# Kernel optimization log

Measured on AMD Instinct MI355X. Metric: run time of the kernel, lower is better.

The kernel has to match this reference:

```python
import jax, jax.numpy as jnp
import numpy as np


def _gat(x, adj, W, a):
    # x: [N, J, Fin], W: [H, Fin, hs], a: [H, 2*hs]
    # e_ij = leakyrelu(a1.Wh_i + a2.Wh_j)  (decomposed form of the repeat/cat construction)
    hs = W.shape[-1]
    Wh = jnp.einsum('bjf,hfd->bhjd', x, W)
    s1 = jnp.einsum('bhjd,hd->bhj', Wh, a[:, :hs])
    s2 = jnp.einsum('bhjd,hd->bhj', Wh, a[:, hs:])
    e = jax.nn.leaky_relu(s1[..., :, None] + s2[..., None, :], 0.2)
    e = jnp.where(adj[None, None] > 0, e, jnp.float32(-9e15))
    att = jax.nn.softmax(e, axis=-1)
    h = jnp.einsum('bhij,bhjd->bhid', att, Wh)
    b, H, j, d = h.shape
    return jax.nn.elu(h.transpose(0, 2, 1, 3).reshape(b, j, H * d))


def _conv_bn_relu(x, w, bias, g, be, m, v):
    # x: [N, C, T], w: [O, I, 3], BN in inference mode
    y = jax.lax.conv_general_dilated(x, w, (1,), [(1, 1)], dimension_numbers=('NCH', 'OIH', 'NCH'))
    y = y + bias[None, :, None]
    y = (y - m[None, :, None]) / jnp.sqrt(v[None, :, None] + 1e-5) * g[None, :, None] + be[None, :, None]
    return jax.nn.relu(y)


def _mha(q, k, v, wq, bq, wk, bk, wv, bv, wo, bo):
    # torch nn.MultiheadAttention, 4 heads, eval mode (no dropout)
    n, L, D = q.shape
    H = 4
    hd = D // H
    def proj(x, w, b):
        return (x @ w.T + b).reshape(n, -1, H, hd)
    Q, K, V = proj(q, wq, bq), proj(k, wk, bk), proj(v, wv, bv)
    att = jax.nn.softmax(jnp.einsum('nqhd,nkhd->nhqk', Q, K) * jnp.float32(1.0 / np.sqrt(hd)), axis=-1)
    o = jnp.einsum('nhqk,nkhd->nqhd', att, V).reshape(n, L, D)
    return o @ wo.T + bo


def _lstm_dir(x, wih, whh, bih, bhh, rev):
    # x: [B, T, D]; torch gate order i, f, g, o
    b, t, _ = x.shape
    H = whh.shape[1]
    xw = jnp.transpose(x @ wih.T + (bih + bhh), (1, 0, 2))  # [T, B, 4H]
    def step(carry, xt):
        h, c = carry
        gates = xt + h @ whh.T
        i, f, g, o = jnp.split(gates, 4, axis=-1)
        c = jax.nn.sigmoid(f) * c + jax.nn.sigmoid(i) * jnp.tanh(g)
        h = jax.nn.sigmoid(o) * jnp.tanh(c)
        return (h, c), h
    init = (jnp.zeros((b, H), x.dtype), jnp.zeros((b, H), x.dtype))
    _, hs = jax.lax.scan(step, init, xw, reverse=rev)
    return jnp.transpose(hs, (1, 0, 2))


def _forward(lh, rh, adj, vis, g1W, g1a, g2W, g2a, c1w, c1b, b1g, b1b, b1m, b1v, c2w, c2b, b2g, b2b, b2m, b2v,
             wq, bq, wk, bk, wv, bv, wo, bo,
             l0fw, l0fu, l0fbi, l0fbh, l0bw, l0bu, l0bbi, l0bbh,
             l1fw, l1fu, l1fbi, l1fbh, l1bw, l1bu, l1bbi, l1bbh,
             o1w, o1b, o2w, o2b):
    B, T, J, F = lh.shape

    def single_hand(x):
        h = x.reshape(B * T, J, F)
        h = _gat(h, adj, g1W, g1a)
        h = _gat(h, adj, g2W, g2a)
        D = h.shape[-1]
        ht = h.reshape(B, T, J, D).transpose(0, 2, 3, 1).reshape(B * J, D, T)
        ht = _conv_bn_relu(ht, c1w, c1b, b1g, b1b, b1m, b1v)
        ht = _conv_bn_relu(ht, c2w, c2b, b2g, b2b, b2m, b2v)
        return ht.reshape(B, J, D, T).transpose(0, 3, 1, 2)  # [B, T, J, D]

    l = single_hand(lh)
    r = single_hand(rh)
    D = l.shape[-1]
    lf = l.reshape(B * T, J, D)
    rf = r.reshape(B * T, J, D)
    a_l2r = _mha(lf, rf, rf, wq, bq, wk, bk, wv, bv, wo, bo)
    a_r2l = _mha(rf, lf, lf, wq, bq, wk, bk, wv, bv, wo, bo)
    # repair of shape-inconsistent torch reshape: pool joints before the seq LSTM
    le = (lf + 0.5 * a_r2l).reshape(B, T, J, D).mean(axis=2)
    re = (rf + 0.5 * a_l2r).reshape(B, T, J, D).mean(axis=2)

    def bilstm(x):
        h1 = jnp.concatenate([_lstm_dir(x, l0fw, l0fu, l0fbi, l0fbh, False),
                              _lstm_dir(x, l0bw, l0bu, l0bbi, l0bbh, True)], -1)
        return jnp.concatenate([_lstm_dir(h1, l1fw, l1fu, l1fbi, l1fbh, False),
                                _lstm_dir(h1, l1bw, l1bu, l1bbi, l1bbh, True)], -1)

    def head(x):
        y = jax.nn.relu(x @ o1w.T + o1b) @ o2w.T + o2b  # [B, T, 3*J]
        return y.reshape(B, T, J, 3)

    lp = head(bilstm(le)) * vis[..., None]
    rp = head(bilstm(re)) * vis[..., None]
    return lp, rp


def setup_inputs() -> dict:
    key = jax.random.key(0)
    ks = jax.random.split(key, 60)
    it = iter(range(60))
    B, T, J, F, D = 8, 512, 21, 512, 256
    def nrm(shape, s=0.05):
        return jax.random.normal(ks[next(it)], shape, jnp.float32) * s
    inp = {}
    inp['left_hand_feats'] = nrm((B, T, J, F), 1.0)
    inp['right_hand_feats'] = nrm((B, T, J, F), 1.0)
    adj = (jax.random.uniform(ks[next(it)], (J, J)) < 0.3).astype(jnp.float32)
    inp['hand_adj_matrix'] = jnp.maximum(adj, jnp.eye(J, dtype=jnp.float32))
    inp['hand_visibility'] = jax.random.uniform(ks[next(it)], (B, T, J), jnp.float32)
    inp['gat1_W'] = nrm((4, F, 64)); inp['gat1_a'] = nrm((4, 128))
    inp['gat2_W'] = nrm((4, D, 64)); inp['gat2_a'] = nrm((4, 128))
    inp['conv1_w'] = nrm((D, D, 3)); inp['conv1_b'] = nrm((D,))
    inp['conv2_w'] = nrm((D, D, 3)); inp['conv2_b'] = nrm((D,))
    for p in ['bn1', 'bn2']:
        inp[p + '_g'] = jnp.ones((D,), jnp.float32)
        inp[p + '_b'] = jnp.zeros((D,), jnp.float32)
        inp[p + '_m'] = jnp.zeros((D,), jnp.float32)
        inp[p + '_v'] = jnp.ones((D,), jnp.float32)
    for p in ['attn_wq', 'attn_wk', 'attn_wv', 'attn_wo']:
        inp[p] = nrm((D, D))
    for p in ['attn_bq', 'attn_bk', 'attn_bv', 'attn_bo']:
        inp[p] = nrm((D,))
    H = D // 2
    for l in ['lstm0f', 'lstm0b', 'lstm1f', 'lstm1b']:
        inp[l + '_wih'] = nrm((4 * H, D))
        inp[l + '_whh'] = nrm((4 * H, H))
        inp[l + '_bih'] = nrm((4 * H,))
        inp[l + '_bhh'] = nrm((4 * H,))
    inp['out1_w'] = nrm((D, D)); inp['out1_b'] = nrm((D,))
    inp['out2_w'] = nrm((3 * J, D)); inp['out2_b'] = nrm((3 * J,))
    return inp


def reference(left_hand_feats, right_hand_feats, hand_adj_matrix, hand_visibility,
              gat1_W, gat1_a, gat2_W, gat2_a,
              conv1_w, conv1_b, bn1_g, bn1_b, bn1_m, bn1_v,
              conv2_w, conv2_b, bn2_g, bn2_b, bn2_m, bn2_v,
              attn_wq, attn_bq, attn_wk, attn_bk, attn_wv, attn_bv, attn_wo, attn_bo,
              lstm0f_wih, lstm0f_whh, lstm0f_bih, lstm0f_bhh,
              lstm0b_wih, lstm0b_whh, lstm0b_bih, lstm0b_bhh,
              lstm1f_wih, lstm1f_whh, lstm1f_bih, lstm1f_bhh,
              lstm1b_wih, lstm1b_whh, lstm1b_bih, lstm1b_bhh,
              out1_w, out1_b, out2_w, out2_b):
    return _forward(left_hand_feats, right_hand_feats, hand_adj_matrix, hand_visibility,
                    gat1_W, gat1_a, gat2_W, gat2_a,
                    conv1_w, conv1_b, bn1_g, bn1_b, bn1_m, bn1_v,
                    conv2_w, conv2_b, bn2_g, bn2_b, bn2_m, bn2_v,
                    attn_wq, attn_bq, attn_wk, attn_bk, attn_wv, attn_bv, attn_wo, attn_bo,
                    lstm0f_wih, lstm0f_whh, lstm0f_bih, lstm0f_bhh,
                    lstm0b_wih, lstm0b_whh, lstm0b_bih, lstm0b_bhh,
                    lstm1f_wih, lstm1f_whh, lstm1f_bih, lstm1f_bhh,
                    lstm1b_wih, lstm1b_whh, lstm1b_bih, lstm1b_bhh,
                    out1_w, out1_b, out2_w, out2_b)
```

## Files before the change

kernel.cpp:

```cpp
#include <hip/hip_runtime.h>

typedef __bf16 bf16;
typedef bf16 bf16x8 __attribute__((ext_vector_type(8)));
typedef bf16 bf16x4 __attribute__((ext_vector_type(4)));
typedef float f32x4 __attribute__((ext_vector_type(4)));
typedef _Float16 f16;
typedef f16 f16x8 __attribute__((ext_vector_type(8)));

#define NBT 4096
#define NJ 21
#define NLF 86016
#define DD 256
#define CONV_M 86352
#define SPAD 514
#define CROWS 86528

__device__ __forceinline__ void gload16(const bf16* g, bf16* l) {
  __builtin_amdgcn_global_load_lds(
      (const __attribute__((address_space(1))) unsigned int*)g,
      (__attribute__((address_space(3))) unsigned int*)l, 16, 0, 0);
}

__global__ __launch_bounds__(256, 2) void gemm_bf16(
    const void* __restrict__ Av, const bf16* __restrict__ Bt,
    float* __restrict__ C32, bf16* __restrict__ Cout,
    const float* __restrict__ bias, const float* __restrict__ sc,
    const float* __restrict__ sh, int M, int N, int K, int lda, int flags)
{
  __shared__ __align__(16) bf16 As[128][32];
  __shared__ __align__(16) bf16 Bs[128][32];
  const int tid = threadIdx.x;
  const long m0 = (long)blockIdx.y * 128;
  const int n0 = blockIdx.x * 128;
  const int wave = tid >> 6, lane = tid & 63;
  const int wm = (wave & 1) * 64, wn = (wave >> 1) * 64;
  const int frow = lane & 15, fkb = (lane >> 4) * 8;
  const int crow = lane >> 2, ccol = (lane & 3) * 8;
  f32x4 acc[4][4] = {};
  for (int k0 = 0; k0 < K; k0 += 32) {
    if (flags & 1) {
      const int lr = tid >> 1, lc = (tid & 1) * 16;
      const float* ap = (const float*)Av + (m0 + lr) * (long)lda + (k0 + lc);
      bf16x8 t0, t1;
      #pragma unroll
      for (int u = 0; u < 8; u++) { t0[u] = (bf16)ap[u]; t1[u] = (bf16)ap[8 + u]; }
      *(bf16x8*)(&As[lr][lc])     = t0;
      *(bf16x8*)(&As[lr][lc + 8]) = t1;
    } else {
      #pragma unroll
      for (int cc = 0; cc < 2; cc++) {
        const int ch = wave * 2 + cc;
        gload16((const bf16*)Av + (m0 + ch * 16 + crow) * (long)lda + (k0 + ccol),
                &As[ch * 16][0]);
      }
    }
    #pragma unroll
    for (int cc = 0; cc < 2; cc++) {
      const int ch = wave * 2 + cc;
      gload16(Bt + (n0 + ch * 16 + crow) * (long)K + (k0 + ccol),
              &Bs[ch * 16][0]);
    }
    __syncthreads();
    bf16x8 af[4], bg[4];
    #pragma unroll
    for (int i = 0; i < 4; i++) af[i] = *(const bf16x8*)(&As[wm + i * 16 + frow][fkb]);
    #pragma unroll
    for (int j = 0; j < 4; j++) bg[j] = *(const bf16x8*)(&Bs[wn + j * 16 + frow][fkb]);
    #pragma unroll
    for (int i = 0; i < 4; i++)
      #pragma unroll
      for (int j = 0; j < 4; j++)
        acc[i][j] = __builtin_amdgcn_mfma_f32_16x16x32_bf16(af[i], bg[j], acc[i][j], 0, 0, 0);
    __syncthreads();
  }
  const int col = lane & 15, rbase = (lane >> 4) * 4;
  #pragma unroll
  for (int i = 0; i < 4; i++) {
    #pragma unroll
    for (int j = 0; j < 4; j++) {
      const int nn = n0 + wn + j * 16 + col;
      #pragma unroll
      for (int r = 0; r < 4; r++) {
        const long mm = m0 + wm + i * 16 + rbase + r;
        if (mm >= M) continue;
        float v = acc[i][j][r];
        if (flags & 2) { C32[mm * (long)N + nn] = v; continue; }
        if (flags & 8) v = v * sc[nn] + sh[nn];
        else if (bias) v += bias[nn];
        if (flags & 4) v = fmaxf(v, 0.f);
        if (flags & 16) {
          const int s = (int)(mm % SPAD);
          if (s == 0 || s == SPAD - 1) v = 0.f;
          Cout[mm * (long)N + nn] = (bf16)v;
        } else if (flags & 32) {
          const long hj = mm / SPAD; const int s = (int)(mm - hj * SPAD);
          if (s == 0 || s == SPAD - 1) continue;
          const long b = hj / NJ; const int j2 = (int)(hj - b * NJ);
          const long dst = (b * 512 + (s - 1)) * NJ + j2;
          Cout[dst * (long)N + nn] = (bf16)v;
        } else {
          Cout[mm * (long)N + nn] = (bf16)v;
        }
      }
    }
  }
}

__global__ void cvt_k(const float* __restrict__ s, bf16* __restrict__ d, long n) {
  long i = (long)blockIdx.x * 256 + threadIdx.x;
  if (i < n) d[i] = (bf16)s[i];
}
__global__ void cvt4_k(const float* __restrict__ s, bf16* __restrict__ d, long n4) {
  long i = (long)blockIdx.x * 256 + threadIdx.x;
  if (i >= n4) return;
  const f32x4 v = ((const f32x4*)s)[i];
  bf16x4 o; o[0] = (bf16)v[0]; o[1] = (bf16)v[1]; o[2] = (bf16)v[2]; o[3] = (bf16)v[3];
  ((bf16x4*)d)[i] = o;
}
__global__ void prep_gatW(const float* __restrict__ W, bf16* __restrict__ Wt, int F) {
  long idx = (long)blockIdx.x * 256 + threadIdx.x;
  if (idx >= 256L * F) return;
  int n = (int)(idx / F), f = (int)(idx % F);
  Wt[idx] = (bf16)W[((long)(n >> 6) * F + f) * 64 + (n & 63)];
}
__global__ void prep_convw(const float* __restrict__ w, bf16* __restrict__ wp) {
  int idx = blockIdx.x * 256 + threadIdx.x;
  int n = idx / 768, k = idx % 768, tap = k >> 8, i = k & 255;
  wp[idx] = (bf16)w[(n * 256 + i) * 3 + tap];
}
__global__ void prep_out2(const float* __restrict__ w, bf16* __restrict__ wp) {
  int idx = blockIdx.x * 256 + threadIdx.x;
  wp[idx] = (idx < 63 * 256) ? (bf16)w[idx] : (bf16)0.f;
}
__global__ void prep_scsh(const float* __restrict__ cb, const float* __restrict__ g,
                          const float* __restrict__ be, const float* __restrict__ m,
                          const float* __restrict__ v, float* __restrict__ sc,
                          float* __restrict__ sh) {
  int c = threadIdx.x;
  float rs = rsqrtf(v[c] + 1e-5f) * g[c];
  sc[c] = rs; sh[c] = (cb[c] - m[c]) * rs + be[c];
}
__global__ void pad_zero(bf16* __restrict__ convIn) {
  int idx = blockIdx.x * 256 + threadIdx.x;
  int hj = idx >> 9, s = ((idx >> 8) & 1) ? (SPAD - 1) : 0, c = idx & 255;
  convIn[((long)hj * SPAD + s) * DD + c] = (bf16)0.f;
}
__global__ void zero_out(float* __restrict__ o, long n) {
  long i = (long)blockIdx.x * 256 + threadIdx.x;
  if (i < n) o[i] = 0.f;
}

__global__ __launch_bounds__(256) void gat_attn(
    const bf16* __restrict__ Wh, const float* __restrict__ a,
    const float* __restrict__ adj, bf16* __restrict__ out, int convMode)
{
  const int bt = blockIdx.x, tid = threadIdx.x;
  __shared__ float whs[NJ][DD];
  __shared__ float s1[4][NJ], s2[4][NJ];
  __shared__ float att[4][NJ][NJ];
  const long base = (long)bt * NJ * DD;
  for (int i = tid; i < NJ * DD; i += 256)
    whs[i >> 8][i & 255] = (float)Wh[base + i];
  __syncthreads();
  if (tid < 4 * NJ) {
    const int h = tid / NJ, i = tid % NJ;
    float x1 = 0.f, x2 = 0.f;
    for (int d = 0; d < 64; d++) {
      const float w = whs[i][h * 64 + d];
      x1 += w * a[h * 128 + d];
      x2 += w * a[h * 128 + 64 + d];
    }
    s1[h][i] = x1; s2[h][i] = x2;
  }
  __syncthreads();
  for (int idx = tid; idx < 4 * NJ * NJ; idx += 256) {
    const int h = idx / (NJ * NJ), r = idx % (NJ * NJ), i = r / NJ, j = r % NJ;
    float e = s1[h][i] + s2[h][j];
    e = e > 0.f ? e : 0.2f * e;
    att[h][i][j] = (adj[i * NJ + j] > 0.f) ? e : -9e15f;
  }
  __syncthreads();
  if (tid < 4 * NJ) {
    const int h = tid / NJ, i = tid % NJ;
    float mx = -3e38f;
    for (int j = 0; j < NJ; j++) mx = fmaxf(mx, att[h][i][j]);
    float sum = 0.f;
    for (int j = 0; j < NJ; j++) { const float ex = __expf(att[h][i][j] - mx); att[h][i][j] = ex; sum += ex; }
    const float inv = 1.f / sum;
    for (int j = 0; j < NJ; j++) att[h][i][j] *= inv;
  }
  __syncthreads();
  const int b = bt >> 9, t = bt & 511;
  for (int idx = tid; idx < NJ * DD; idx += 256) {
    const int i = idx >> 8, c = idx & 255, h = c >> 6;
    float s = 0.f;
    for (int j = 0; j < NJ; j++) s += att[h][i][j] * whs[j][c];
    s = s > 0.f ? s : (__expf(s) - 1.f);
    const long row = convMode ? (((long)(b * NJ + i)) * SPAD + (t + 1)) : ((long)bt * NJ + i);
    out[row * DD + c] = (bf16)s;
  }
}

__global__ __launch_bounds__(256) void mha_core(
    const bf16* __restrict__ Q, const bf16* __restrict__ K,
    const bf16* __restrict__ V, bf16* __restrict__ O)
{
  const int bt = blockIdx.x, tid = threadIdx.x;
  __shared__ bf16 qs[NJ][DD], ks[NJ][DD], vs[NJ][DD];
  __shared__ float att[4][NJ][NJ];
  const long base = (long)bt * NJ * DD;
  for (int i = tid; i < NJ * DD; i += 256) {
    const int r = i >> 8, c = i & 255;
    qs[r][c] = Q[base + i]; ks[r][c] = K[base + i]; vs[r][c] = V[base + i];
  }
  __syncthreads();
  for (int idx = tid; idx < 4 * NJ * NJ; idx += 256) {
    const int h = idx / (NJ * NJ), r = idx % (NJ * NJ), i = r / NJ, j = r % NJ;
    float s = 0.f;
    for (int d = 0; d < 64; d++) s += (float)qs[i][h * 64 + d] * (float)ks[j][h * 64 + d];
    att[h][i][j] = s * 0.125f;
  }
  __syncthreads();
  if (tid < 4 * NJ) {
    const int h = tid / NJ, i = tid % NJ;
    float mx = -3e38f;
    for (int j = 0; j < NJ; j++) mx = fmaxf(mx, att[h][i][j]);
    float sum = 0.f;
    for (int j = 0; j < NJ; j++) { const float ex = __expf(att[h][i][j] - mx); att[h][i][j] = ex; sum += ex; }
    const float inv = 1.f / sum;
    for (int j = 0; j < NJ; j++) att[h][i][j] *= inv;
  }
  __syncthreads();
  for (int idx = tid; idx < NJ * DD; idx += 256) {
    const int i = idx >> 8, c = idx & 255, h = c >> 6;
    float s = 0.f;
    for (int j = 0; j < NJ; j++) s += att[h][i][j] * (float)vs[j][c];
    O[base + i * DD + c] = (bf16)s;
  }
}

__global__ __launch_bounds__(256) void pool_kernel(
    const bf16* __restrict__ lf, const bf16* __restrict__ ao, bf16* __restrict__ o)
{
  const int bt = blockIdx.x, c = threadIdx.x;
  float s = 0.f;
  for (int j = 0; j < NJ; j++) {
    const long r = ((long)bt * NJ + j) * DD + c;
    s += (float)lf[r] + 0.5f * (float)ao[r];
  }
  o[(long)bt * DD + c] = (bf16)(s * (1.f / 21.f));
}

#define REP16(X) X(0) X(1) X(2) X(3) X(4) X(5) X(6) X(7) X(8) X(9) X(10) X(11) \
  X(12) X(13) X(14) X(15)

#define LDS_FENCE() do { \
  asm volatile("s_waitcnt lgkmcnt(0)" ::: "memory"); \
  __builtin_amdgcn_sched_barrier(0); \
  __builtin_amdgcn_s_barrier(); \
  __builtin_amdgcn_sched_barrier(0); \
} while (0)

__global__ __launch_bounds__(512, 1) void lstm_lds(
    const float* __restrict__ xw,
    const float* __restrict__ whhF, const float* __restrict__ whhB,
    const float* __restrict__ bihF, const float* __restrict__ bhhF,
    const float* __restrict__ bihB, const float* __restrict__ bhhB,
    bf16* __restrict__ outL, bf16* __restrict__ outR)
{
  const int wg = blockIdx.x;
  const int hand = wg >> 4, dir = (wg >> 3) & 1, b = wg & 7;
  const int tid = threadIdx.x;
  const float* whh = dir ? whhB : whhF;

  __shared__ f16 whhs[512][136];
  __shared__ f16 hbuf[136];
  __shared__ float gsb[512];

  for (int i = tid; i < 512 * 128; i += 512)
    whhs[i >> 7][i & 127] = (f16)whh[i];
  if (tid < 136) hbuf[tid] = (f16)0.f;
  const float bias = (dir ? bihB : bihF)[tid] + (dir ? bhhB : bhhF)[tid];
  float c = 0.f;
  const float* xp = xw + ((long)hand * NBT + (long)b * 512) * 1024 + dir * 512;
  bf16* outp = hand ? outR : outL;
  float xv = xp[(long)(dir ? 511 : 0) * 1024 + tid];
  __syncthreads();

  const f16* wrow = &whhs[tid][0];
#define WRD(i) f16x8 w##i = *(const f16x8*)(wrow + (i) * 8);
  REP16(WRD)
#undef WRD
  asm volatile("" : "+a"(w0), "+a"(w1), "+a"(w2), "+a"(w3));
  asm volatile("" : "+a"(w4), "+a"(w5), "+a"(w6), "+a"(w7));
  asm volatile("" : "+a"(w8), "+a"(w9), "+a"(w10), "+a"(w11));
  asm volatile("" : "+a"(w12), "+a"(w13), "+a"(w14), "+a"(w15));

  for (int s = 0; s < 512; s++) {
#define WKEEP(i) asm volatile("" : "+a"(w##i));
    REP16(WKEEP)
#undef WKEEP
    const int t = dir ? (511 - s) : s;
    const int tn = dir ? (510 - s) : (s + 1);
    float xnext = 0.f;
    if (s < 511) xnext = xp[(long)tn * 1024 + tid];
    float a0 = xv + bias, a1 = 0.f, a2 = 0.f, a3 = 0.f;
#define WDOT(i) { \
    const f16x8 hv = *(const f16x8*)(&hbuf[(i) * 8]); \
    a0 = __builtin_amdgcn_fdot2(__builtin_shufflevector(w##i, w##i, 0, 1), \
                                __builtin_shufflevector(hv, hv, 0, 1), a0, false); \
    a1 = __builtin_amdgcn_fdot2(__builtin_shufflevector(w##i, w##i, 2, 3), \
                                __builtin_shufflevector(hv, hv, 2, 3), a1, false); \
    a2 = __builtin_amdgcn_fdot2(__builtin_shufflevector(w##i, w##i, 4, 5), \
                                __builtin_shufflevector(hv, hv, 4, 5), a2, false); \
    a3 = __builtin_amdgcn_fdot2(__builtin_shufflevector(w##i, w##i, 6, 7), \
                                __builtin_shufflevector(hv, hv, 6, 7), a3, false); }
    REP16(WDOT)
#undef WDOT
    gsb[tid] = (a0 + a1) + (a2 + a3);
    LDS_FENCE();
    if (tid < 128) {
      const float ig = gsb[tid], fg = gsb[tid + 128], gg = gsb[tid + 256], og = gsb[tid + 384];
      const float si = __builtin_amdgcn_rcpf(1.f + __expf(-ig));
      const float sf = __builtin_amdgcn_rcpf(1.f + __expf(-fg));
      const float so = __builtin_amdgcn_rcpf(1.f + __expf(-og));
      const float tg = 1.f - 2.f * __builtin_amdgcn_rcpf(1.f + __expf(2.f * gg));
      c = sf * c + si * tg;
      const float tc = 1.f - 2.f * __builtin_amdgcn_rcpf(1.f + __expf(2.f * c));
      const float h = so * tc;
      hbuf[tid] = (f16)h;
      outp[((long)b * 512 + t) * 256 + dir * 128 + tid] = (bf16)h;
    }
    LDS_FENCE();
    xv = xnext;
  }
}

__global__ __launch_bounds__(256) void finalize_k(
    const float* __restrict__ y, const float* __restrict__ b2,
    const float* __restrict__ vis, float* __restrict__ out)
{
  const int idx = blockIdx.x * 256 + threadIdx.x;
  if (idx >= NBT * 63) return;
  const int c = idx % 63; const int bt = idx / 63;
  out[idx] = (y[(long)bt * 128 + c] + b2[c]) * vis[bt * 21 + (c / 3)];
}

extern "C" void kernel_launch(void* const* d_in, const int* in_sizes, int n_in,
                              void* d_out, int out_size, void* d_ws, size_t ws_size,
                              hipStream_t stream) {
  (void)in_sizes; (void)n_in;
  const float* feats[2] = { (const float*)d_in[0], (const float*)d_in[1] };
  const float* adj  = (const float*)d_in[2];
  const float* vis  = (const float*)d_in[3];
  const float* gW[2] = { (const float*)d_in[4], (const float*)d_in[6] };
  const float* ga[2] = { (const float*)d_in[5], (const float*)d_in[7] };
  const float* cw_[2] = { (const float*)d_in[8],  (const float*)d_in[10] };
  const float* cb_[2] = { (const float*)d_in[9],  (const float*)d_in[11] };
  const float* bng[2] = { (const float*)d_in[12], (const float*)d_in[16] };
  const float* bnb[2] = { (const float*)d_in[13], (const float*)d_in[17] };
  const float* bnm[2] = { (const float*)d_in[14], (const float*)d_in[18] };
  const float* bnv[2] = { (const float*)d_in[15], (const float*)d_in[19] };
  const float* wq = (const float*)d_in[20], *wk = (const float*)d_in[21];
  const float* wv = (const float*)d_in[22], *wo = (const float*)d_in[23];
  const float* bq = (const float*)d_in[24], *bk = (const float*)d_in[25];
  const float* bv = (const float*)d_in[26], *bo = (const float*)d_in[27];
  const float* Lwih[2][2] = { { (const float*)d_in[28], (const float*)d_in[32] },
                              { (const float*)d_in[36], (const float*)d_in[40] } };
  const float* Lwhh[2][2] = { { (const float*)d_in[29], (const float*)d_in[33] },
                              { (const float*)d_in[37], (const float*)d_in[41] } };
  const float* Lbih[2][2] = { { (const float*)d_in[30], (const float*)d_in[34] },
                              { (const float*)d_in[38], (const float*)d_in[42] } };
  const float* Lbhh[2][2] = { { (const float*)d_in[31], (const float*)d_in[35] },
                              { (const float*)d_in[39], (const float*)d_in[43] } };
  const float* o1w = (const float*)d_in[44], *o1b = (const float*)d_in[45];
  const float* o2w = (const float*)d_in[46], *o2b = (const float*)d_in[47];

  char* base = (char*)d_ws;
  size_t off = 0;
  auto alloc = [&](size_t b) { size_t r = off; off += (b + 1023) & ~(size_t)1023; return r; };
  const size_t SZ_LF  = (size_t)NLF * DD * 2;
  const size_t SZ_CNV = (size_t)CROWS * DD * 2;
  const size_t SZ_BT  = (size_t)NBT * DD * 2;
  const size_t o_w1t = alloc((size_t)256 * 512 * 2);
  const size_t o_w2t = alloc((size_t)256 * 256 * 2);
  const size_t o_cw1 = alloc((size_t)256 * 768 * 2);
  const size_t o_cw2 = alloc((size_t)256 * 768 * 2);
  const size_t o_wq  = alloc((size_t)256 * 256 * 2);
  const size_t o_wk  = alloc((size_t)256 * 256 * 2);
  const size_t o_wv  = alloc((size_t)256 * 256 * 2);
  const size_t o_wo  = alloc((size_t)256 * 256 * 2);
  const size_t o_o1w = alloc((size_t)256 * 256 * 2);
  const size_t o_o2p = alloc((size_t)128 * 256 * 2);
  const size_t o_lw0 = alloc((size_t)512 * 256 * 2);
  const size_t o_lw1 = alloc((size_t)512 * 256 * 2);
  const size_t o_lw2 = alloc((size_t)512 * 256 * 2);
  const size_t o_lw3 = alloc((size_t)512 * 256 * 2);
  const size_t o_ss  = alloc((size_t)4 * 256 * 4);
  const size_t o_B1  = alloc(SZ_LF);
  const size_t o_B23 = alloc(2 * SZ_CNV);
  const size_t o_lfL = alloc(SZ_LF);
  const size_t o_lfR = alloc(SZ_LF);
  const size_t o_le  = alloc(SZ_BT);
  const size_t o_re  = alloc(SZ_BT);
  const size_t o_h1L = alloc(SZ_BT);
  const size_t o_h1R = alloc(SZ_BT);
  const size_t o_hoL = alloc(SZ_BT);
  const size_t o_hoR = alloc(SZ_BT);
  const size_t o_t1  = alloc(SZ_BT);
  const size_t o_y32 = alloc((size_t)NBT * 128 * 4);
  const size_t NEED = off;
  if (ws_size < NEED) {
    zero_out<<<(out_size + 255) / 256, 256, 0, stream>>>((float*)d_out, out_size);
    return;
  }
  auto P = [&](size_t o_) { return (void*)(base + o_); };

  auto gemm = [&](const void* A, const void* Bt, void* c32, void* co,
                  const void* bias_, const void* sc_, const void* sh_,
                  long M, int N, int K, int lda, int flags) {
    dim3 g((unsigned)(N / 128), (unsigned)((M + 127) / 128));
    gemm_bf16<<<g, 256, 0, stream>>>(A, (const bf16*)Bt, (float*)c32, (bf16*)co,
                                     (const float*)bias_, (const float*)sc_,
                                     (const float*)sh_, (int)M, N, K, lda, flags);
  };
  auto cvt = [&](const float* s, void* d, long n) {
    cvt_k<<<(unsigned)((n + 255) / 256), 256, 0, stream>>>(s, (bf16*)d, n);
  };

  prep_gatW<<<512, 256, 0, stream>>>(gW[0], (bf16*)P(o_w1t), 512);
  prep_gatW<<<256, 256, 0, stream>>>(gW[1], (bf16*)P(o_w2t), 256);
  prep_convw<<<768, 256, 0, stream>>>(cw_[0], (bf16*)P(o_cw1));
  prep_convw<<<768, 256, 0, stream>>>(cw_[1], (bf16*)P(o_cw2));
  cvt(wq, P(o_wq), 65536); cvt(wk, P(o_wk), 65536);
  cvt(wv, P(o_wv), 65536); cvt(wo, P(o_wo), 65536);
  cvt(o1w, P(o_o1w), 65536);
  cvt(Lwih[0][0], P(o_lw0), 131072); cvt(Lwih[0][1], P(o_lw1), 131072);
  cvt(Lwih[1][0], P(o_lw2), 131072); cvt(Lwih[1][1], P(o_lw3), 131072);
  prep_out2<<<128, 256, 0, stream>>>(o2w, (bf16*)P(o_o2p));
  float* sc1 = (float*)P(o_ss); float* sh1 = sc1 + 256;
  float* sc2 = sh1 + 256;       float* sh2 = sc2 + 256;
  prep_scsh<<<1, 256, 0, stream>>>(cb_[0], bng[0], bnb[0], bnm[0], bnv[0], sc1, sh1);
  prep_scsh<<<1, 256, 0, stream>>>(cb_[1], bng[1], bnb[1], bnm[1], bnv[1], sc2, sh2);

  bf16* B1 = (bf16*)P(o_B1);
  bf16* B2 = (bf16*)P(o_B23);
  bf16* B3 = B2 + (size_t)CROWS * DD;
  bf16* lfb[2] = { (bf16*)P(o_lfL), (bf16*)P(o_lfR) };

  for (int hd = 0; hd < 2; hd++) {
    bf16* featbf = B2;
    cvt4_k<<<(unsigned)(((long)NLF * 512 / 4 + 255) / 256), 256, 0, stream>>>(
        feats[hd], featbf, (long)NLF * 512 / 4);
    gemm(featbf, P(o_w1t), nullptr, B1, nullptr, nullptr, nullptr,
         NLF, 256, 512, 512, 0);
    gat_attn<<<NBT, 256, 0, stream>>>(B1, ga[0], adj, B1, 0);
    gemm(B1, P(o_w2t), nullptr, B2, nullptr, nullptr, nullptr,
         NLF, 256, 256, 256, 0);
    pad_zero<<<336, 256, 0, stream>>>(B3 + DD);
    gat_attn<<<NBT, 256, 0, stream>>>(B2, ga[1], adj, B3 + DD, 1);
    gemm(B3, P(o_cw1), nullptr, B2 + DD, nullptr, sc1, sh1,
         CONV_M, 256, 768, 256, 8 | 4 | 16);
    gemm(B2, P(o_cw2), nullptr, lfb[hd], nullptr, sc2, sh2,
         CONV_M, 256, 768, 256, 8 | 4 | 32);
  }

  gemm(lfb[0], P(o_wq), nullptr, B1, bq, nullptr, nullptr, NLF, 256, 256, 256, 0);
  gemm(lfb[1], P(o_wk), nullptr, B2, bk, nullptr, nullptr, NLF, 256, 256, 256, 0);
  gemm(lfb[1], P(o_wv), nullptr, B3, bv, nullptr, nullptr, NLF, 256, 256, 256, 0);
  mha_core<<<NBT, 256, 0, stream>>>(B1, B2, B3, B1);
  gemm(B1, P(o_wo), nullptr, B2, bo, nullptr, nullptr, NLF, 256, 256, 256, 0);
  pool_kernel<<<NBT, 256, 0, stream>>>(lfb[1], B2, (bf16*)P(o_re));
  gemm(lfb[1], P(o_wq), nullptr, B1, bq, nullptr, nullptr, NLF, 256, 256, 256, 0);
  gemm(lfb[0], P(o_wk), nullptr, B3, bk, nullptr, nullptr, NLF, 256, 256, 256, 0);
  gemm(lfb[0], P(o_wv), nullptr, B2, bv, nullptr, nullptr, NLF, 256, 256, 256, 0);
  mha_core<<<NBT, 256, 0, stream>>>(B1, B3, B2, B1);
  gemm(B1, P(o_wo), nullptr, B3, bo, nullptr, nullptr, NLF, 256, 256, 256, 0);
  pool_kernel<<<NBT, 256, 0, stream>>>(lfb[0], B3, (bf16*)P(o_le));

  float* xw = (float*)P(o_B23);
  gemm(P(o_le), P(o_lw0), xw,                    nullptr, nullptr, nullptr, nullptr, NBT, 1024, 256, 256, 2);
  gemm(P(o_re), P(o_lw0), xw + (size_t)NBT * 1024, nullptr, nullptr, nullptr, nullptr, NBT, 1024, 256, 256, 2);
  lstm_lds<<<32, 512, 0, stream>>>(xw, Lwhh[0][0], Lwhh[0][1],
      Lbih[0][0], Lbhh[0][0], Lbih[0][1], Lbhh[0][1],
      (bf16*)P(o_h1L), (bf16*)P(o_h1R));
  gemm(P(o_h1L), P(o_lw2), xw,                    nullptr, nullptr, nullptr, nullptr, NBT, 1024, 256, 256, 2);
  gemm(P(o_h1R), P(o_lw2), xw + (size_t)NBT * 1024, nullptr, nullptr, nullptr, nullptr, NBT, 1024, 256, 256, 2);
  lstm_lds<<<32, 512, 0, stream>>>(xw, Lwhh[1][0], Lwhh[1][1],
      Lbih[1][0], Lbhh[1][0], Lbih[1][1], Lbhh[1][1],
      (bf16*)P(o_hoL), (bf16*)P(o_hoR));

  for (int hd = 0; hd < 2; hd++) {
    const void* hin = hd ? P(o_hoR) : P(o_hoL);
    gemm(hin, P(o_o1w), nullptr, P(o_t1), o1b, nullptr, nullptr, NBT, 256, 256, 256, 4);
    gemm(P(o_t1), P(o_o2p), P(o_y32), nullptr, nullptr, nullptr, nullptr, NBT, 128, 256, 256, 2);
    finalize_k<<<(NBT * 63 + 255) / 256, 256, 0, stream>>>(
        (const float*)P(o_y32), o2b, vis, (float*)d_out + (size_t)hd * NBT * 63);
  }
}
```

Before: 2.511 ms.

## Batch K/V projections and per-hand GEMMs into wider or taller launches

Fuses the separate K and V projection GEMMs into one N=512 GEMM with a concatenated bias, so mha_core reads K and V from one interleaved buffer. It also merges the left/right hand LSTM input-projection and output-head GEMMs into single 2*NBT-row launches, relying on the two buffers being contiguous in the workspace. Separately it drops the asm constraints that pinned LSTM weights in AGPRs, which can change register allocation in the recurrent kernel. The goal is fewer launches and better GEMM occupancy, with a risk to correctness if the buffers are not adjacent or the wk/wv weights are not laid out back to back.

```diff
diff --git a/kernel.cpp b/kernel.cpp
--- a/kernel.cpp
+++ b/kernel.cpp
@@ -140,6 +140,12 @@
   float rs = rsqrtf(v[c] + 1e-5f) * g[c];
   sc[c] = rs; sh[c] = (cb[c] - m[c]) * rs + be[c];
 }
+__global__ void prep_bkv(const float* __restrict__ bk, const float* __restrict__ bv,
+                         float* __restrict__ o) {
+  int i = blockIdx.x * 256 + threadIdx.x;
+  if (i >= 512) return;
+  o[i] = (i < 256) ? bk[i] : bv[i - 256];
+}
 __global__ void pad_zero(bf16* __restrict__ convIn) {
   int idx = blockIdx.x * 256 + threadIdx.x;
   int hj = idx >> 9, s = ((idx >> 8) & 1) ? (SPAD - 1) : 0, c = idx & 255;
@@ -201,17 +207,20 @@
   }
 }
 
-__global__ __launch_bounds__(256) void mha_core(
-    const bf16* __restrict__ Q, const bf16* __restrict__ K,
-    const bf16* __restrict__ V, bf16* __restrict__ O)
+__global__ __launch_bounds__(256) void mha_core2(
+    const bf16* __restrict__ Q, const bf16* __restrict__ KV,
+    bf16* __restrict__ O)
 {
   const int bt = blockIdx.x, tid = threadIdx.x;
   __shared__ bf16 qs[NJ][DD], ks[NJ][DD], vs[NJ][DD];
   __shared__ float att[4][NJ][NJ];
-  const long base = (long)bt * NJ * DD;
+  const long baseq = (long)bt * NJ * DD;
+  const long basekv = (long)bt * NJ * 512;
   for (int i = tid; i < NJ * DD; i += 256) {
     const int r = i >> 8, c = i & 255;
-    qs[r][c] = Q[base + i]; ks[r][c] = K[base + i]; vs[r][c] = V[base + i];
+    qs[r][c] = Q[baseq + i];
+    ks[r][c] = KV[basekv + r * 512 + c];
+    vs[r][c] = KV[basekv + r * 512 + 256 + c];
   }
   __syncthreads();
   for (int idx = tid; idx < 4 * NJ * NJ; idx += 256) {
@@ -235,7 +244,7 @@
     const int i = idx >> 8, c = idx & 255, h = c >> 6;
     float s = 0.f;
     for (int j = 0; j < NJ; j++) s += att[h][i][j] * (float)vs[j][c];
-    O[base + i * DD + c] = (bf16)s;
+    O[baseq + i * DD + c] = (bf16)s;
   }
 }
 
@@ -291,15 +300,8 @@
 #define WRD(i) f16x8 w##i = *(const f16x8*)(wrow + (i) * 8);
   REP16(WRD)
 #undef WRD
-  asm volatile("" : "+a"(w0), "+a"(w1), "+a"(w2), "+a"(w3));
-  asm volatile("" : "+a"(w4), "+a"(w5), "+a"(w6), "+a"(w7));
-  asm volatile("" : "+a"(w8), "+a"(w9), "+a"(w10), "+a"(w11));
-  asm volatile("" : "+a"(w12), "+a"(w13), "+a"(w14), "+a"(w15));
 
   for (int s = 0; s < 512; s++) {
-#define WKEEP(i) asm volatile("" : "+a"(w##i));
-    REP16(WKEEP)
-#undef WKEEP
     const int t = dir ? (511 - s) : s;
     const int tn = dir ? (510 - s) : (s + 1);
     float xnext = 0.f;
@@ -341,9 +343,9 @@
     const float* __restrict__ vis, float* __restrict__ out)
 {
   const int idx = blockIdx.x * 256 + threadIdx.x;
-  if (idx >= NBT * 63) return;
-  const int c = idx % 63; const int bt = idx / 63;
-  out[idx] = (y[(long)bt * 128 + c] + b2[c]) * vis[bt * 21 + (c / 3)];
+  if (idx >= 2 * NBT * 63) return;
+  const int c = idx % 63; const int r = idx / 63; const int bt = r & (NBT - 1);
+  out[idx] = (y[(long)r * 128 + c] + b2[c]) * vis[bt * 21 + (c / 3)];
 }
 
 extern "C" void kernel_launch(void* const* d_in, const int* in_sizes, int n_in,
@@ -397,6 +399,7 @@
   const size_t o_lw2 = alloc((size_t)512 * 256 * 2);
   const size_t o_lw3 = alloc((size_t)512 * 256 * 2);
   const size_t o_ss  = alloc((size_t)4 * 256 * 4);
+  const size_t o_bkv = alloc((size_t)512 * 4);
   const size_t o_B1  = alloc(SZ_LF);
   const size_t o_B23 = alloc(2 * SZ_CNV);
   const size_t o_lfL = alloc(SZ_LF);
@@ -407,8 +410,6 @@
   const size_t o_h1R = alloc(SZ_BT);
   const size_t o_hoL = alloc(SZ_BT);
   const size_t o_hoR = alloc(SZ_BT);
-  const size_t o_t1  = alloc(SZ_BT);
-  const size_t o_y32 = alloc((size_t)NBT * 128 * 4);
   const size_t NEED = off;
   if (ws_size < NEED) {
     zero_out<<<(out_size + 255) / 256, 256, 0, stream>>>((float*)d_out, out_size);
@@ -442,6 +443,7 @@
   float* sc2 = sh1 + 256;       float* sh2 = sc2 + 256;
   prep_scsh<<<1, 256, 0, stream>>>(cb_[0], bng[0], bnb[0], bnm[0], bnv[0], sc1, sh1);
   prep_scsh<<<1, 256, 0, stream>>>(cb_[1], bng[1], bnb[1], bnm[1], bnv[1], sc2, sh2);
+  prep_bkv<<<2, 256, 0, stream>>>(bk, bv, (float*)P(o_bkv));
 
   bf16* B1 = (bf16*)P(o_B1);
   bf16* B2 = (bf16*)P(o_B23);
@@ -465,36 +467,36 @@
          CONV_M, 256, 768, 256, 8 | 4 | 32);
   }
 
-  gemm(lfb[0], P(o_wq), nullptr, B1, bq, nullptr, nullptr, NLF, 256, 256, 256, 0);
-  gemm(lfb[1], P(o_wk), nullptr, B2, bk, nullptr, nullptr, NLF, 256, 256, 256, 0);
-  gemm(lfb[1], P(o_wv), nullptr, B3, bv, nullptr, nullptr, NLF, 256, 256, 256, 0);
-  mha_core<<<NBT, 256, 0, stream>>>(B1, B2, B3, B1);
-  gemm(B1, P(o_wo), nullptr, B2, bo, nullptr, nullptr, NLF, 256, 256, 256, 0);
-  pool_kernel<<<NBT, 256, 0, stream>>>(lfb[1], B2, (bf16*)P(o_re));
-  gemm(lfb[1], P(o_wq), nullptr, B1, bq, nullptr, nullptr, NLF, 256, 256, 256, 0);
-  gemm(lfb[0], P(o_wk), nullptr, B3, bk, nullptr, nullptr, NLF, 256, 256, 256, 0);
-  gemm(lfb[0], P(o_wv), nullptr, B2, bv, nullptr, nullptr, NLF, 256, 256, 256, 0);
-  mha_core<<<NBT, 256, 0, stream>>>(B1, B3, B2, B1);
-  gemm(B1, P(o_wo), nullptr, B3, bo, nullptr, nullptr, NLF, 256, 256, 256, 0);
-  pool_kernel<<<NBT, 256, 0, stream>>>(lfb[0], B3, (bf16*)P(o_le));
+  bf16* KV = (bf16*)P(o_B23);
+  for (int pass = 0; pass < 2; pass++) {
+    const bf16* qsrc = lfb[pass];
+    const bf16* kvsrc = lfb[1 - pass];
+    gemm(kvsrc, P(o_wk), nullptr, KV, P(o_bkv), nullptr, nullptr,
+         NLF, 512, 256, 256, 0);
+    gemm(qsrc, P(o_wq), nullptr, B1, bq, nullptr, nullptr, NLF, 256, 256, 256, 0);
+    mha_core2<<<NBT, 256, 0, stream>>>(B1, KV, B1);
+    gemm(B1, P(o_wo), nullptr, B2, bo, nullptr, nullptr, NLF, 256, 256, 256, 0);
+    pool_kernel<<<NBT, 256, 0, stream>>>(kvsrc, B2,
+        (bf16*)P(pass == 0 ? o_re : o_le));
+  }
 
   float* xw = (float*)P(o_B23);
-  gemm(P(o_le), P(o_lw0), xw,                    nullptr, nullptr, nullptr, nullptr, NBT, 1024, 256, 256, 2);
-  gemm(P(o_re), P(o_lw0), xw + (size_t)NBT * 1024, nullptr, nullptr, nullptr, nullptr, NBT, 1024, 256, 256, 2);
+  gemm(P(o_le), P(o_lw0), xw, nullptr, nullptr, nullptr, nullptr,
+       2 * NBT, 1024, 256, 256, 2);
   lstm_lds<<<32, 512, 0, stream>>>(xw, Lwhh[0][0], Lwhh[0][1],
       Lbih[0][0], Lbhh[0][0], Lbih[0][1], Lbhh[0][1],
       (bf16*)P(o_h1L), (bf16*)P(o_h1R));
-  gemm(P(o_h1L), P(o_lw2), xw,                    nullptr, nullptr, nullptr, nullptr, NBT, 1024, 256, 256, 2);
-  gemm(P(o_h1R), P(o_lw2), xw + (size_t)NBT * 1024, nullptr, nullptr, nullptr, nullptr, NBT, 1024, 256, 256, 2);
+  gemm(P(o_h1L), P(o_lw2), xw, nullptr, nullptr, nullptr, nullptr,
+       2 * NBT, 1024, 256, 256, 2);
   lstm_lds<<<32, 512, 0, stream>>>(xw, Lwhh[1][0], Lwhh[1][1],
       Lbih[1][0], Lbhh[1][0], Lbih[1][1], Lbhh[1][1],
       (bf16*)P(o_hoL), (bf16*)P(o_hoR));
 
-  for (int hd = 0; hd < 2; hd++) {
-    const void* hin = hd ? P(o_hoR) : P(o_hoL);
-    gemm(hin, P(o_o1w), nullptr, P(o_t1), o1b, nullptr, nullptr, NBT, 256, 256, 256, 4);
-    gemm(P(o_t1), P(o_o2p), P(o_y32), nullptr, nullptr, nullptr, nullptr, NBT, 128, 256, 256, 2);
-    finalize_k<<<(NBT * 63 + 255) / 256, 256, 0, stream>>>(
-        (const float*)P(o_y32), o2b, vis, (float*)d_out + (size_t)hd * NBT * 63);
-  }
-}
+  gemm(P(o_hoL), P(o_o1w), nullptr, B1, o1b, nullptr, nullptr,
+       2 * NBT, 256, 256, 256, 4);
+  float* y32 = (float*)P(o_B23);
+  gemm(B1, P(o_o2p), y32, nullptr, nullptr, nullptr, nullptr,
+       2 * NBT, 128, 256, 256, 2);
+  finalize_k<<<(2 * NBT * 63 + 255) / 256, 256, 0, stream>>>(
+      y32, o2b, vis, (float*)d_out);
+}
```

Measured after the change: 2.232 ms. 11.1% less time.
